# Optimization experiments

Measured on AMD Instinct MI355X. Metric: run time of the kernel, lower is better.

The kernel has to match this reference:

```python
import jax, jax.numpy as jnp
import numpy as np

NUM_NODES = 50000
NUM_EDGES = 800000
IN_CH = 128
HID = 128
NUM_LAYERS = 3
CONF_HID = 64
TAU0 = 1.0


def _glorot(key, shape):
    lim = (6.0 / (shape[0] + shape[1])) ** 0.5
    return jax.random.uniform(key, shape, jnp.float32, -lim, lim)


def setup_inputs() -> dict:
    key = jax.random.key(0)
    ks = jax.random.split(key, 16)
    inp = {
        "x": jax.random.normal(ks[0], (NUM_NODES, IN_CH), jnp.float32),
        "edge_index": jax.random.randint(ks[1], (2, NUM_EDGES), 0, NUM_NODES, jnp.int32),
    }
    dims = [(IN_CH, HID)] + [(HID, HID)] * (NUM_LAYERS - 1)
    for i, (di, do) in enumerate(dims):
        inp[f"conv_w{i}"] = _glorot(ks[2 + i], (di, do))
        inp[f"conv_b{i}"] = jnp.zeros((do,), jnp.float32)
    inp["conf_w1"] = _glorot(ks[8], (HID, CONF_HID))
    inp["conf_b1"] = jnp.zeros((CONF_HID,), jnp.float32)
    inp["conf_w2"] = _glorot(ks[9], (CONF_HID, 2))
    inp["conf_b2"] = jnp.zeros((2,), jnp.float32)
    inp["temp_w"] = _glorot(ks[10], (HID, 1))
    return inp


def _gcn_conv(x, W, b, src, dst):
    # PyG GCNConv: linear -> add self loops -> sym-normalized aggregate -> bias
    h = x @ W
    loop = jnp.arange(NUM_NODES, dtype=src.dtype)
    s = jnp.concatenate([src, loop])
    d = jnp.concatenate([dst, loop])
    deg = jax.ops.segment_sum(jnp.ones(d.shape, h.dtype), d, num_segments=NUM_NODES)
    dinv = jnp.where(deg > 0, deg ** -0.5, 0.0)
    norm = dinv[s] * dinv[d]  # [E+N]
    out = jax.ops.segment_sum(h[s] * norm[:, None], d, num_segments=NUM_NODES)
    return out + b


def _forward(x, edge_index, conv_ws, conv_bs, conf_w1, conf_b1, conf_w2, conf_b2, temp_w):
    src, dst = edge_index[0], edge_index[1]
    gkey = jax.random.key(42)
    z = jnp.zeros((NUM_NODES, HID), jnp.float32)
    continue_mask = jnp.ones((NUM_NODES,), bool)
    exit_layers = jnp.full((NUM_NODES,), NUM_LAYERS, jnp.int32)
    active = []
    for layer_idx in range(NUM_LAYERS):
        x = _gcn_conv(x, conv_ws[layer_idx], conv_bs[layer_idx], src, dst)
        if layer_idx < NUM_LAYERS - 1:
            x = jax.nn.gelu(x, approximate=False)  # eval mode: dropout is identity
        active.append(jnp.sum(continue_mask).astype(jnp.int32))
        logits = jax.nn.relu(x @ conf_w1 + conf_b1) @ conf_w2 + conf_b2  # [N,2]
        temp = 1.0 / (jax.nn.softplus(x @ temp_w) + TAU0)  # [N,1], always finite
        u = jax.random.uniform(jax.random.fold_in(gkey, layer_idx), logits.shape,
                               jnp.float32, 1e-10, 1.0)
        gumbels = -jnp.log(-jnp.log(u))
        y = jax.nn.softmax((logits + gumbels) / temp, axis=-1)
        exit_decision = y[:, 1] > y[:, 0]
        newly_exited = exit_decision & continue_mask
        z = z + x * newly_exited[:, None].astype(x.dtype)
        exit_layers = jnp.where(newly_exited, layer_idx, exit_layers)
        continue_mask = continue_mask & ~exit_decision
    z = z + x * continue_mask[:, None].astype(x.dtype)
    return z, exit_layers, jnp.stack(active)


def reference(x, edge_index, conv_w0, conv_b0, conv_w1, conv_b1, conv_w2, conv_b2,
              conf_w1, conf_b1, conf_w2, conf_b2, temp_w):
    return _forward(x, edge_index,
                    [conv_w0, conv_w1, conv_w2], [conv_b0, conv_b1, conv_b2],
                    conf_w1, conf_b1, conf_w2, conf_b2, temp_w)
```

## Files before the change

kernel.cpp:

```cpp
#include <hip/hip_runtime.h>
#include <stdint.h>

#define NN 50000
#define NE 800000
#define CH 128

typedef double d4 __attribute__((ext_vector_type(4)));

__host__ __device__ inline void tf2x32(uint32_t k0, uint32_t k1, uint32_t& x0, uint32_t& x1) {
  uint32_t ks2 = k0 ^ k1 ^ 0x1BD11BDAu;
  x0 += k0; x1 += k1;
#define ROTL(v, r) (((v) << (r)) | ((v) >> (32 - (r))))
#define RND(r) { x0 += x1; x1 = ROTL(x1, r); x1 ^= x0; }
  RND(13) RND(15) RND(26) RND(6)
  x0 += k1; x1 += ks2 + 1u;
  RND(17) RND(29) RND(16) RND(24)
  x0 += ks2; x1 += k0 + 2u;
  RND(13) RND(15) RND(26) RND(6)
  x0 += k0; x1 += k1 + 3u;
  RND(17) RND(29) RND(16) RND(24)
  x0 += k1; x1 += ks2 + 4u;
  RND(13) RND(15) RND(26) RND(6)
  x0 += ks2; x1 += k0 + 5u;
#undef RND
#undef ROTL
}

__device__ inline float bits_to_u(uint32_t b) {
  float f = __uint_as_float(0x3F800000u | (b >> 9)) - 1.0f;
  f = f + 1e-10f;
  return fmaxf(1e-10f, f);
}

__global__ __launch_bounds__(256) void deg_k(const int* __restrict__ dst, int* __restrict__ degi) {
  int i = blockIdx.x * 256 + threadIdx.x;
  if (i < NE) atomicAdd(&degi[dst[i]], 1);
}

__global__ __launch_bounds__(256) void scan1_k(const int* __restrict__ degi, int* __restrict__ offs,
                                               int* __restrict__ part, float* __restrict__ dinv) {
  __shared__ int tmp[256];
  int t = threadIdx.x, b = blockIdx.x, i = b * 256 + t;
  int v = (i < NN) ? degi[i] : 0;
  tmp[t] = v;
  __syncthreads();
  for (int s = 1; s < 256; s <<= 1) {
    int a = (t >= s) ? tmp[t - s] : 0;
    __syncthreads();
    tmp[t] += a;
    __syncthreads();
  }
  int incl = tmp[t];
  if (i < NN) {
    offs[i] = incl - v;
    dinv[i] = 1.0f / sqrtf((float)(v + 1));
  }
  if (t == 255) part[b] = incl;
}

__global__ void scan2_k(int* part, int nparts) {
  if (threadIdx.x == 0 && blockIdx.x == 0) {
    int run = 0;
    for (int i = 0; i < nparts; ++i) { int v = part[i]; part[i] = run; run += v; }
  }
}

__global__ __launch_bounds__(256) void scan3_k(int* __restrict__ offs, const int* __restrict__ part) {
  int i = blockIdx.x * 256 + threadIdx.x;
  if (i < NN) offs[i] += part[blockIdx.x];
  if (i == 0) offs[NN] = NE;
}

__global__ __launch_bounds__(256) void place_k(const int* __restrict__ src, const int* __restrict__ dst,
                                               const int* __restrict__ offs,
                                               int* __restrict__ cnt, int* __restrict__ srcs) {
  int i = blockIdx.x * 256 + threadIdx.x;
  if (i < NE) {
    int d = dst[i];
    int p = offs[d] + atomicAdd(&cnt[d], 1);
    srcs[p] = src[i];
  }
}

__global__ __launch_bounds__(256) void gum_k(float* __restrict__ gum, float* __restrict__ eout,
                                             uint32_t k00, uint32_t k01, uint32_t k10, uint32_t k11,
                                             uint32_t k20, uint32_t k21) {
  int i = blockIdx.x * 256 + threadIdx.x;
  if (i >= 3 * NN) return;
  if (i < NN) eout[i] = 3.0f;
  int l = i / NN;
  int n = i - l * NN;
  uint32_t kx, ky;
  if (l == 0) { kx = k00; ky = k01; }
  else if (l == 1) { kx = k10; ky = k11; }
  else { kx = k20; ky = k21; }
  int j0 = 2 * n, j1 = 2 * n + 1;
  uint32_t w0, w1;
  if (j0 < NN) {
    uint32_t a0 = (uint32_t)j0, a1 = (uint32_t)(j0 + NN);
    tf2x32(kx, ky, a0, a1); w0 = a0;
    uint32_t b0 = (uint32_t)j1, b1 = (uint32_t)(j1 + NN);
    tf2x32(kx, ky, b0, b1); w1 = b0;
  } else {
    uint32_t a0 = (uint32_t)(j0 - NN), a1 = (uint32_t)j0;
    tf2x32(kx, ky, a0, a1); w0 = a1;
    uint32_t b0 = (uint32_t)(j1 - NN), b1 = (uint32_t)j1;
    tf2x32(kx, ky, b0, b1); w1 = b1;
  }
  float u0 = bits_to_u(w0), u1 = bits_to_u(w1);
  gum[2 * (size_t)i]     = -logf(-logf(u0));
  gum[2 * (size_t)i + 1] = -logf(-logf(u1));
}

__global__ __launch_bounds__(256) void lin_k(const float* __restrict__ x, const float* __restrict__ W,
                                             float* __restrict__ h) {
  __shared__ float Ws[32 * 128];
  __shared__ float xs[64][36];
  int t = threadIdx.x;
  int row0 = blockIdx.x << 6;
  int tr = t & 15, tc = t >> 4;
  float4 acc[4][2];
#pragma unroll
  for (int i = 0; i < 4; ++i) { acc[i][0] = make_float4(0,0,0,0); acc[i][1] = make_float4(0,0,0,0); }

  for (int kt = 0; kt < 4; ++kt) {
    __syncthreads();
    {
      const float4* W4 = (const float4*)(W + (size_t)(kt * 32) * 128);
      float4* Ws4 = (float4*)Ws;
#pragma unroll
      for (int i = 0; i < 4; ++i) Ws4[t + 256 * i] = W4[t + 256 * i];
    }
    {
#pragma unroll
      for (int i = 0; i < 2; ++i) {
        int f = t + 256 * i;
        int row = f >> 3, c4 = f & 7;
        int gr = row0 + row;
        float4 v = make_float4(0,0,0,0);
        if (gr < NN) v = ((const float4*)x)[(size_t)gr * 32 + kt * 8 + c4];
        *(float4*)&xs[row][4 * c4] = v;
      }
    }
    __syncthreads();
    const float4* Ws4 = (const float4*)Ws;
#pragma unroll
    for (int kk = 0; kk < 32; kk += 4) {
      float4 xv[4];
#pragma unroll
      for (int i = 0; i < 4; ++i) xv[i] = *(const float4*)&xs[tr + 16 * i][kk];
#pragma unroll
      for (int d = 0; d < 4; ++d) {
        float4 w0 = Ws4[(kk + d) * 32 + tc];
        float4 w1 = Ws4[(kk + d) * 32 + 16 + tc];
#pragma unroll
        for (int i = 0; i < 4; ++i) {
          float xd = ((const float*)&xv[i])[d];
          acc[i][0].x += xd * w0.x; acc[i][0].y += xd * w0.y;
          acc[i][0].z += xd * w0.z; acc[i][0].w += xd * w0.w;
          acc[i][1].x += xd * w1.x; acc[i][1].y += xd * w1.y;
          acc[i][1].z += xd * w1.z; acc[i][1].w += xd * w1.w;
        }
      }
    }
  }
#pragma unroll
  for (int i = 0; i < 4; ++i) {
    int gr = row0 + tr + 16 * i;
    if (gr < NN) {
      ((float4*)h)[(size_t)gr * 32 + tc] = acc[i][0];
      ((float4*)h)[(size_t)gr * 32 + 16 + tc] = acc[i][1];
    }
  }
}

__device__ inline float gelu_exact(float v) {
  return 0.5f * v * (1.0f + erff(v / 1.4142135623730951f));
}

__global__ __launch_bounds__(256) void agg_k(const float* __restrict__ h, const float* __restrict__ dinv,
                                             const int* __restrict__ offs, const int* __restrict__ srcs,
                                             const float* __restrict__ bias,
                                             float* __restrict__ xout, int act) {
  int lane = threadIdx.x & 63, w = threadIdx.x >> 6;
  int n = blockIdx.x * 4 + w;
  if (n >= NN) return;
  int c4 = lane & 31, hh = lane >> 5;
  int s0 = offs[n], s1 = offs[n + 1];
  float dv = dinv[n];
  double a0 = 0.0, a1 = 0.0, a2 = 0.0, a3 = 0.0;
  for (int p0 = s0; p0 < s1; p0 += 64) {
    int m = s1 - p0; if (m > 64) m = 64;
    int sv = 0; float nv = 0.f;
    if (lane < m) {
      sv = __builtin_nontemporal_load(&srcs[p0 + lane]);
      nv = dinv[sv] * dv;
    }
    int i = 0;
    for (; i + 8 <= m; i += 8) {
      int   sA = __shfl(sv, i + hh),     sB = __shfl(sv, i + 2 + hh);
      int   sC = __shfl(sv, i + 4 + hh), sD = __shfl(sv, i + 6 + hh);
      float nA = __shfl(nv, i + hh),     nB = __shfl(nv, i + 2 + hh);
      float nC = __shfl(nv, i + 4 + hh), nD = __shfl(nv, i + 6 + hh);
      float4 hA = *(const float4*)&h[(size_t)sA * CH + 4 * c4];
      float4 hB = *(const float4*)&h[(size_t)sB * CH + 4 * c4];
      float4 hC = *(const float4*)&h[(size_t)sC * CH + 4 * c4];
      float4 hD = *(const float4*)&h[(size_t)sD * CH + 4 * c4];
      a0 += (double)(hA.x * nA); a1 += (double)(hA.y * nA); a2 += (double)(hA.z * nA); a3 += (double)(hA.w * nA);
      a0 += (double)(hB.x * nB); a1 += (double)(hB.y * nB); a2 += (double)(hB.z * nB); a3 += (double)(hB.w * nB);
      a0 += (double)(hC.x * nC); a1 += (double)(hC.y * nC); a2 += (double)(hC.z * nC); a3 += (double)(hC.w * nC);
      a0 += (double)(hD.x * nD); a1 += (double)(hD.y * nD); a2 += (double)(hD.z * nD); a3 += (double)(hD.w * nD);
    }
    for (; i < m; i += 2) {
      int   s = __shfl(sv, i + hh);
      float nm = __shfl(nv, i + hh);
      float4 hv = *(const float4*)&h[(size_t)s * CH + 4 * c4];
      a0 += (double)(hv.x * nm); a1 += (double)(hv.y * nm); a2 += (double)(hv.z * nm); a3 += (double)(hv.w * nm);
    }
  }
  a0 += __shfl_xor(a0, 32); a1 += __shfl_xor(a1, 32);
  a2 += __shfl_xor(a2, 32); a3 += __shfl_xor(a3, 32);
  if (hh == 0) {
    float selfn = dv * dv;
    float4 hn = *(const float4*)&h[(size_t)n * CH + 4 * c4];
    a0 += (double)(hn.x * selfn); a1 += (double)(hn.y * selfn);
    a2 += (double)(hn.z * selfn); a3 += (double)(hn.w * selfn);
    float4 bv = *(const float4*)&bias[4 * c4];
    float r0 = (float)a0 + bv.x;
    float r1 = (float)a1 + bv.y;
    float r2 = (float)a2 + bv.z;
    float r3 = (float)a3 + bv.w;
    if (act) { r0 = gelu_exact(r0); r1 = gelu_exact(r1); r2 = gelu_exact(r2); r3 = gelu_exact(r3); }
    float4 o; o.x = r0; o.y = r1; o.z = r2; o.w = r3;
    *(float4*)&xout[(size_t)n * CH + 4 * c4] = o;
  }
}

template <int MODE>
__global__ __launch_bounds__(256) void decide_k(const float* __restrict__ x, const float* __restrict__ W1,
                                                const float* __restrict__ b1, const float* __restrict__ W2,
                                                const float* __restrict__ b2, const float* __restrict__ gum,
                                                float* __restrict__ zout, float* __restrict__ eout,
                                                float layerf) {
  __shared__ float b1s[64];
  __shared__ float w2s[128];
  __shared__ float b2s[2];
  __shared__ float xs[4][16][132];
  int t = threadIdx.x;
  if (t < 64) b1s[t] = b1[t];
  if (t < 128) w2s[t] = W2[t];
  if (t < 2) b2s[t] = b2[t];

  int lane = t & 63, w = t >> 6;
  int n0 = blockIdx.x * 64 + w * 16;
#pragma unroll
  for (int i = 0; i < 8; ++i) {
    int f = lane + 64 * i;
    int row = f >> 5, c4 = f & 31;
    int gr = n0 + row;
    float4 v = make_float4(0.f, 0.f, 0.f, 0.f);
    if (gr < NN) v = ((const float4*)x)[(size_t)gr * 32 + c4];
    *(float4*)&xs[w][row][4 * c4] = v;
  }

  int g = lane >> 4, r = lane & 15;
  bool writer = (r < 4);
  int mynode = n0 + 4 * g + r;
  float ev = 3.0f;
  float gg0 = 0.f, gg1 = 0.f;
  if (writer && mynode < NN) {
    if (MODE > 0) ev = eout[mynode];
    gg0 = gum[2 * (size_t)mynode];
    gg1 = gum[2 * (size_t)mynode + 1];
  }
  bool m_act = writer && (mynode < NN) && (MODE == 0 || ev == 3.0f);
  unsigned long long actmask = __ballot(m_act);
  __syncthreads();
  if (MODE > 0 && actmask == 0ULL) return;

  d4 acc0 = {0., 0., 0., 0.}, acc1 = {0., 0., 0., 0.};
  d4 acc2 = {0., 0., 0., 0.}, acc3 = {0., 0., 0., 0.};
#pragma unroll 4
  for (int ks = 0; ks < 32; ++ks) {
    int k = 4 * ks + g;
    double av = (double)xs[w][r][k];
    const float* Wk = W1 + (size_t)k * 64;
    double b0 = (double)Wk[r];
    double b1v = (double)Wk[16 + r];
    double b2v = (double)Wk[32 + r];
    double b3v = (double)Wk[48 + r];
    acc0 = __builtin_amdgcn_mfma_f64_16x16x4f64(av, b0, acc0, 0, 0, 0);
    acc1 = __builtin_amdgcn_mfma_f64_16x16x4f64(av, b1v, acc1, 0, 0, 0);
    acc2 = __builtin_amdgcn_mfma_f64_16x16x4f64(av, b2v, acc2, 0, 0, 0);
    acc3 = __builtin_amdgcn_mfma_f64_16x16x4f64(av, b3v, acc3, 0, 0, 0);
  }

  double p0[4], p1[4];
#pragma unroll
  for (int i = 0; i < 4; ++i) {
    float h0 = fmaxf((float)acc0[i] + b1s[r], 0.f);
    float h1 = fmaxf((float)acc1[i] + b1s[16 + r], 0.f);
    float h2 = fmaxf((float)acc2[i] + b1s[32 + r], 0.f);
    float h3 = fmaxf((float)acc3[i] + b1s[48 + r], 0.f);
    double q0 = (double)h0 * (double)w2s[2 * r] + (double)h1 * (double)w2s[2 * (16 + r)] +
                (double)h2 * (double)w2s[2 * (32 + r)] + (double)h3 * (double)w2s[2 * (48 + r)];
    double q1 = (double)h0 * (double)w2s[2 * r + 1] + (double)h1 * (double)w2s[2 * (16 + r) + 1] +
                (double)h2 * (double)w2s[2 * (32 + r) + 1] + (double)h3 * (double)w2s[2 * (48 + r) + 1];
#pragma unroll
    for (int off = 1; off <= 8; off <<= 1) {
      q0 += __shfl_xor(q0, off);
      q1 += __shfl_xor(q1, off);
    }
    p0[i] = q0; p1[i] = q1;
  }

  double q0sel = p0[0], q1sel = p1[0];
  if (r == 1) { q0sel = p0[1]; q1sel = p1[1]; }
  if (r == 2) { q0sel = p0[2]; q1sel = p1[2]; }
  if (r == 3) { q0sel = p0[3]; q1sel = p1[3]; }
  bool myex = false;
  if (writer && mynode < NN) {
    float l0 = (float)q0sel + b2s[0];
    float l1 = (float)q1sel + b2s[1];
    myex = (l1 + gg1) > (l0 + gg0);
  }
  unsigned long long exmask = __ballot(myex);

  if (m_act && myex) eout[mynode] = layerf;

#pragma unroll
  for (int i = 0; i < 16; ++i) {
    int bitpos = 16 * (i >> 2) + (i & 3);
    bool a = (actmask >> bitpos) & 1ULL;
    bool ee = (exmask >> bitpos) & 1ULL;
    if (a && (MODE == 2 || ee)) {
      int node = n0 + i;
      float2 v;
      v.x = xs[w][i][2 * lane];
      v.y = xs[w][i][2 * lane + 1];
      *(float2*)&zout[(size_t)node * CH + 2 * lane] = v;
    }
  }
}

__global__ __launch_bounds__(1024) void cnt_k(const float* __restrict__ eout, float* __restrict__ aout) {
  __shared__ int s1[16], s2[16];
  int t = threadIdx.x;
  int c1 = 0, c2 = 0;
  for (int i = t; i < NN / 4; i += 1024) {
    float4 v = ((const float4*)eout)[i];
    c1 += (v.x < 0.5f) + (v.y < 0.5f) + (v.z < 0.5f) + (v.w < 0.5f);
    c2 += (v.x < 1.5f) + (v.y < 1.5f) + (v.z < 1.5f) + (v.w < 1.5f);
  }
#pragma unroll
  for (int off = 32; off >= 1; off >>= 1) { c1 += __shfl_xor(c1, off); c2 += __shfl_xor(c2, off); }
  if ((t & 63) == 0) { s1[t >> 6] = c1; s2[t >> 6] = c2; }
  __syncthreads();
  if (t == 0) {
    int a1 = 0, a2 = 0;
#pragma unroll
    for (int i = 0; i < 16; ++i) { a1 += s1[i]; a2 += s2[i]; }
    aout[0] = 50000.0f;
    aout[1] = (float)(NN - a1);
    aout[2] = (float)(NN - a2);
  }
}

extern "C" void kernel_launch(void* const* d_in, const int* in_sizes, int n_in,
                              void* d_out, int out_size, void* d_ws, size_t ws_size,
                              hipStream_t stream) {
  const float* x_in = (const float*)d_in[0];
  const int* eidx = (const int*)d_in[1];
  const int* esrc = eidx;
  const int* edst = eidx + NE;
  const float* convw[3] = {(const float*)d_in[2], (const float*)d_in[4], (const float*)d_in[6]};
  const float* convb[3] = {(const float*)d_in[3], (const float*)d_in[5], (const float*)d_in[7]};
  const float* cw1 = (const float*)d_in[8];
  const float* cb1 = (const float*)d_in[9];
  const float* cw2 = (const float*)d_in[10];
  const float* cb2 = (const float*)d_in[11];

  float* out = (float*)d_out;
  float* zout = out;
  float* eout = out + (size_t)NN * CH;
  float* aout = eout + NN;

  char* w = (char*)d_ws;
  float* P = (float*)w;   w += (size_t)NN * CH * 4;
  float* Q = (float*)w;   w += (size_t)NN * CH * 4;
  int* srcs = (int*)w;    w += (size_t)NE * 4;
  float* gum = (float*)w; w += (size_t)3 * NN * 2 * 4;
  int* offs = (int*)w;    w += (size_t)(NN + 1) * 4;
  float* dinv = (float*)w; w += (size_t)NN * 4;
  char* zr0 = w;
  int* degi = (int*)w;    w += (size_t)NN * 4;
  int* cnt = (int*)w;     w += (size_t)NN * 4;
  int* parts = (int*)w;   w += 1024;

  hipMemsetAsync(zr0, 0, (size_t)(2 * NN) * 4, stream);

  uint32_t key[3][2];
  for (int l = 0; l < 3; ++l) {
    uint32_t a = 0u, b = (uint32_t)l;
    tf2x32(0u, 42u, a, b);
    key[l][0] = a; key[l][1] = b;
  }

  const int nblkN = (NN + 255) / 256;
  deg_k<<<(NE + 255) / 256, 256, 0, stream>>>(edst, degi);
  scan1_k<<<nblkN, 256, 0, stream>>>(degi, offs, parts, dinv);
  scan2_k<<<1, 64, 0, stream>>>(parts, nblkN);
  scan3_k<<<nblkN, 256, 0, stream>>>(offs, parts);
  place_k<<<(NE + 255) / 256, 256, 0, stream>>>(esrc, edst, offs, cnt, srcs);
  gum_k<<<(3 * NN + 255) / 256, 256, 0, stream>>>(gum, eout, key[0][0], key[0][1], key[1][0], key[1][1],
                                                  key[2][0], key[2][1]);

  const int LB = (NN + 63) / 64;
  const int AB = (NN + 3) / 4;
  const int DB = (NN + 63) / 64;
  for (int l = 0; l < 3; ++l) {
    const float* xin = (l == 0) ? x_in : Q;
    lin_k<<<LB, 256, 0, stream>>>(xin, convw[l], P);
    agg_k<<<AB, 256, 0, stream>>>(P, dinv, offs, srcs, convb[l], Q, (l < 2) ? 1 : 0);
    if (l == 0)
      decide_k<0><<<DB, 256, 0, stream>>>(Q, cw1, cb1, cw2, cb2, gum, zout, eout, 0.0f);
    else if (l == 1)
      decide_k<1><<<DB, 256, 0, stream>>>(Q, cw1, cb1, cw2, cb2, gum + (size_t)NN * 2, zout, eout, 1.0f);
    else
      decide_k<2><<<DB, 256, 0, stream>>>(Q, cw1, cb1, cw2, cb2, gum + (size_t)2 * NN * 2, zout, eout, 2.0f);
  }
  cnt_k<<<1, 1024, 0, stream>>>(eout, aout);
}
```

Before: 466.3 us.

## Fuse exit-decision MLP into GCN aggregation kernel, one wave per node

Removes the separate decide kernel and computes the confidence MLP, Gumbel decision and z/exit writes at the end of the aggregation kernel. Each wave stages its own output row in LDS and evaluates the 128x64 hidden layer with per-lane fp64 FMAs instead of fp64 MFMA tiles. This drops three kernel launches and avoids re-reading the full activation matrix each layer. In exchange, the aggregation kernel gets longer, has more register and LDS pressure, and re-loads W1 from cache in every wave.

New measurement: 464.4 us. No clear change (-0.4%).

```diff
diff --git a/kernel.cpp b/kernel.cpp
--- a/kernel.cpp
+++ b/kernel.cpp
@@ -4,8 +4,6 @@
 #define NN 50000
 #define NE 800000
 #define CH 128
-
-typedef double d4 __attribute__((ext_vector_type(4)));
 
 __host__ __device__ inline void tf2x32(uint32_t k0, uint32_t k1, uint32_t& x0, uint32_t& x1) {
   uint32_t ks2 = k0 ^ k1 ^ 0x1BD11BDAu;
@@ -178,10 +176,16 @@
   return 0.5f * v * (1.0f + erff(v / 1.4142135623730951f));
 }
 
+template <int MODE>
 __global__ __launch_bounds__(256) void agg_k(const float* __restrict__ h, const float* __restrict__ dinv,
                                              const int* __restrict__ offs, const int* __restrict__ srcs,
                                              const float* __restrict__ bias,
-                                             float* __restrict__ xout, int act) {
+                                             const float* __restrict__ W1, const float* __restrict__ b1,
+                                             const float* __restrict__ W2, const float* __restrict__ b2,
+                                             const float* __restrict__ gum,
+                                             float* __restrict__ xout, float* __restrict__ zout,
+                                             float* __restrict__ eout) {
+  __shared__ float xrow[4][128];
   int lane = threadIdx.x & 63, w = threadIdx.x >> 6;
   int n = blockIdx.x * 4 + w;
   if (n >= NN) return;
@@ -230,116 +234,47 @@
     float r1 = (float)a1 + bv.y;
     float r2 = (float)a2 + bv.z;
     float r3 = (float)a3 + bv.w;
-    if (act) { r0 = gelu_exact(r0); r1 = gelu_exact(r1); r2 = gelu_exact(r2); r3 = gelu_exact(r3); }
+    if (MODE < 2) { r0 = gelu_exact(r0); r1 = gelu_exact(r1); r2 = gelu_exact(r2); r3 = gelu_exact(r3); }
     float4 o; o.x = r0; o.y = r1; o.z = r2; o.w = r3;
     *(float4*)&xout[(size_t)n * CH + 4 * c4] = o;
-  }
-}
-
-template <int MODE>
-__global__ __launch_bounds__(256) void decide_k(const float* __restrict__ x, const float* __restrict__ W1,
-                                                const float* __restrict__ b1, const float* __restrict__ W2,
-                                                const float* __restrict__ b2, const float* __restrict__ gum,
-                                                float* __restrict__ zout, float* __restrict__ eout,
-                                                float layerf) {
-  __shared__ float b1s[64];
-  __shared__ float w2s[128];
-  __shared__ float b2s[2];
-  __shared__ float xs[4][16][132];
-  int t = threadIdx.x;
-  if (t < 64) b1s[t] = b1[t];
-  if (t < 128) w2s[t] = W2[t];
-  if (t < 2) b2s[t] = b2[t];
-
-  int lane = t & 63, w = t >> 6;
-  int n0 = blockIdx.x * 64 + w * 16;
-#pragma unroll
-  for (int i = 0; i < 8; ++i) {
-    int f = lane + 64 * i;
-    int row = f >> 5, c4 = f & 31;
-    int gr = n0 + row;
-    float4 v = make_float4(0.f, 0.f, 0.f, 0.f);
-    if (gr < NN) v = ((const float4*)x)[(size_t)gr * 32 + c4];
-    *(float4*)&xs[w][row][4 * c4] = v;
-  }
-
-  int g = lane >> 4, r = lane & 15;
-  bool writer = (r < 4);
-  int mynode = n0 + 4 * g + r;
+    *(float4*)&xrow[w][4 * c4] = o;
+  }
+
   float ev = 3.0f;
-  float gg0 = 0.f, gg1 = 0.f;
-  if (writer && mynode < NN) {
-    if (MODE > 0) ev = eout[mynode];
-    gg0 = gum[2 * (size_t)mynode];
-    gg1 = gum[2 * (size_t)mynode + 1];
-  }
-  bool m_act = writer && (mynode < NN) && (MODE == 0 || ev == 3.0f);
-  unsigned long long actmask = __ballot(m_act);
-  __syncthreads();
-  if (MODE > 0 && actmask == 0ULL) return;
-
-  d4 acc0 = {0., 0., 0., 0.}, acc1 = {0., 0., 0., 0.};
-  d4 acc2 = {0., 0., 0., 0.}, acc3 = {0., 0., 0., 0.};
-#pragma unroll 4
-  for (int ks = 0; ks < 32; ++ks) {
-    int k = 4 * ks + g;
-    double av = (double)xs[w][r][k];
-    const float* Wk = W1 + (size_t)k * 64;
-    double b0 = (double)Wk[r];
-    double b1v = (double)Wk[16 + r];
-    double b2v = (double)Wk[32 + r];
-    double b3v = (double)Wk[48 + r];
-    acc0 = __builtin_amdgcn_mfma_f64_16x16x4f64(av, b0, acc0, 0, 0, 0);
-    acc1 = __builtin_amdgcn_mfma_f64_16x16x4f64(av, b1v, acc1, 0, 0, 0);
-    acc2 = __builtin_amdgcn_mfma_f64_16x16x4f64(av, b2v, acc2, 0, 0, 0);
-    acc3 = __builtin_amdgcn_mfma_f64_16x16x4f64(av, b3v, acc3, 0, 0, 0);
-  }
-
-  double p0[4], p1[4];
-#pragma unroll
-  for (int i = 0; i < 4; ++i) {
-    float h0 = fmaxf((float)acc0[i] + b1s[r], 0.f);
-    float h1 = fmaxf((float)acc1[i] + b1s[16 + r], 0.f);
-    float h2 = fmaxf((float)acc2[i] + b1s[32 + r], 0.f);
-    float h3 = fmaxf((float)acc3[i] + b1s[48 + r], 0.f);
-    double q0 = (double)h0 * (double)w2s[2 * r] + (double)h1 * (double)w2s[2 * (16 + r)] +
-                (double)h2 * (double)w2s[2 * (32 + r)] + (double)h3 * (double)w2s[2 * (48 + r)];
-    double q1 = (double)h0 * (double)w2s[2 * r + 1] + (double)h1 * (double)w2s[2 * (16 + r) + 1] +
-                (double)h2 * (double)w2s[2 * (32 + r) + 1] + (double)h3 * (double)w2s[2 * (48 + r) + 1];
-#pragma unroll
-    for (int off = 1; off <= 8; off <<= 1) {
-      q0 += __shfl_xor(q0, off);
-      q1 += __shfl_xor(q1, off);
-    }
-    p0[i] = q0; p1[i] = q1;
-  }
-
-  double q0sel = p0[0], q1sel = p1[0];
-  if (r == 1) { q0sel = p0[1]; q1sel = p1[1]; }
-  if (r == 2) { q0sel = p0[2]; q1sel = p1[2]; }
-  if (r == 3) { q0sel = p0[3]; q1sel = p1[3]; }
-  bool myex = false;
-  if (writer && mynode < NN) {
-    float l0 = (float)q0sel + b2s[0];
-    float l1 = (float)q1sel + b2s[1];
-    myex = (l1 + gg1) > (l0 + gg0);
-  }
-  unsigned long long exmask = __ballot(myex);
-
-  if (m_act && myex) eout[mynode] = layerf;
-
-#pragma unroll
-  for (int i = 0; i < 16; ++i) {
-    int bitpos = 16 * (i >> 2) + (i & 3);
-    bool a = (actmask >> bitpos) & 1ULL;
-    bool ee = (exmask >> bitpos) & 1ULL;
-    if (a && (MODE == 2 || ee)) {
-      int node = n0 + i;
-      float2 v;
-      v.x = xs[w][i][2 * lane];
-      v.y = xs[w][i][2 * lane + 1];
-      *(float2*)&zout[(size_t)node * CH + 2 * lane] = v;
-    }
+  if (MODE > 0) ev = eout[n];
+  bool doDec = (MODE == 0) || (ev == 3.0f);
+  if (!doDec) return;
+
+  double c0 = 0.0, c1 = 0.0, c2 = 0.0, c3 = 0.0;
+  const float* xr = xrow[w];
+#pragma unroll 8
+  for (int k = 0; k < 128; k += 4) {
+    c0 += (double)xr[k]     * (double)W1[(size_t)(k)     * 64 + lane];
+    c1 += (double)xr[k + 1] * (double)W1[(size_t)(k + 1) * 64 + lane];
+    c2 += (double)xr[k + 2] * (double)W1[(size_t)(k + 2) * 64 + lane];
+    c3 += (double)xr[k + 3] * (double)W1[(size_t)(k + 3) * 64 + lane];
+  }
+  double accd = (c0 + c1) + (c2 + c3);
+  float hid = fmaxf((float)accd + b1[lane], 0.0f);
+  double p0 = (double)hid * (double)W2[2 * lane];
+  double p1 = (double)hid * (double)W2[2 * lane + 1];
+#pragma unroll
+  for (int off = 32; off >= 1; off >>= 1) {
+    p0 += __shfl_xor(p0, off);
+    p1 += __shfl_xor(p1, off);
+  }
+  float gg0 = gum[2 * (size_t)n];
+  float gg1 = gum[2 * (size_t)n + 1];
+  float l0 = (float)p0 + b2[0];
+  float l1 = (float)p1 + b2[1];
+  bool ex = (l1 + gg1) > (l0 + gg0);
+
+  if (ex && lane == 0) eout[n] = (float)MODE;
+  if (MODE == 2 || ex) {
+    float2 v;
+    v.x = xr[2 * lane];
+    v.y = xr[2 * lane + 1];
+    *(float2*)&zout[(size_t)n * CH + 2 * lane] = v;
   }
 }
 
@@ -417,17 +352,14 @@
 
   const int LB = (NN + 63) / 64;
   const int AB = (NN + 3) / 4;
-  const int DB = (NN + 63) / 64;
-  for (int l = 0; l < 3; ++l) {
-    const float* xin = (l == 0) ? x_in : Q;
-    lin_k<<<LB, 256, 0, stream>>>(xin, convw[l], P);
-    agg_k<<<AB, 256, 0, stream>>>(P, dinv, offs, srcs, convb[l], Q, (l < 2) ? 1 : 0);
-    if (l == 0)
-      decide_k<0><<<DB, 256, 0, stream>>>(Q, cw1, cb1, cw2, cb2, gum, zout, eout, 0.0f);
-    else if (l == 1)
-      decide_k<1><<<DB, 256, 0, stream>>>(Q, cw1, cb1, cw2, cb2, gum + (size_t)NN * 2, zout, eout, 1.0f);
-    else
-      decide_k<2><<<DB, 256, 0, stream>>>(Q, cw1, cb1, cw2, cb2, gum + (size_t)2 * NN * 2, zout, eout, 2.0f);
-  }
+  lin_k<<<LB, 256, 0, stream>>>(x_in, convw[0], P);
+  agg_k<0><<<AB, 256, 0, stream>>>(P, dinv, offs, srcs, convb[0], cw1, cb1, cw2, cb2,
+                                   gum, Q, zout, eout);
+  lin_k<<<LB, 256, 0, stream>>>(Q, convw[1], P);
+  agg_k<1><<<AB, 256, 0, stream>>>(P, dinv, offs, srcs, convb[1], cw1, cb1, cw2, cb2,
+                                   gum + (size_t)NN * 2, Q, zout, eout);
+  lin_k<<<LB, 256, 0, stream>>>(Q, convw[2], P);
+  agg_k<2><<<AB, 256, 0, stream>>>(P, dinv, offs, srcs, convb[2], cw1, cb1, cw2, cb2,
+                                   gum + (size_t)2 * NN * 2, Q, zout, eout);
   cnt_k<<<1, 1024, 0, stream>>>(eout, aout);
 }
```
